# Performance work log

Hardware: AMD Instinct MI355X
Metric: run time of the kernel (lower is better)

The kernel has to match this reference:

```python
import jax, jax.numpy as jnp
import numpy as np

SIM_THRESHOLD = 0.7
EPS = 1e-8  # matches torch F.cosine_similarity eps

Q, M, D, C = 4096, 65536, 384, 128


def setup_inputs() -> dict:
    key = jax.random.key(0)
    k1, k2, k3 = jax.random.split(key, 3)
    query_embeddings = jax.random.normal(k1, (Q, D), dtype=jnp.float32)
    memory_embeddings = jax.random.normal(k2, (M, D), dtype=jnp.float32)
    # per-example one-hot-ish label vectors [M, C]
    memory_labels = jax.random.uniform(k3, (M, C), dtype=jnp.float32)
    return {
        "query_embeddings": query_embeddings,
        "memory_embeddings": memory_embeddings,
        "memory_labels": memory_labels,
    }


def _l2_normalize(x):
    n = jnp.sqrt(jnp.sum(x * x, axis=-1, keepdims=True))
    return x / jnp.maximum(n, EPS)


def reference(query_embeddings, memory_embeddings, memory_labels):
    # cosine similarity matrix [Q, M] via normalized GEMM
    qn = _l2_normalize(query_embeddings)          # [Q, D]
    mn = _l2_normalize(memory_embeddings)         # [M, D]
    sims = jnp.einsum("qd,md->qm", qn, mn)        # [Q, M]
    max_sim = jnp.max(sims, axis=1)               # [Q]
    max_idx = jnp.argmax(sims, axis=1)            # [Q]
    picked = memory_labels[max_idx]               # [Q, C] gather
    C_ = memory_labels.shape[1]
    uniform = jnp.full((1, C_), 1.0 / C_, dtype=picked.dtype)
    predictions = jnp.where((max_sim > SIM_THRESHOLD)[:, None], picked, uniform)
    return predictions
```

## Files before the change

### kernel.cpp

```cpp
#include <hip/hip_runtime.h>
#include <math.h>

#define QN 4096
#define MN 65536
#define DN 384
#define CN 128
#define NCHUNK 64
#define MROWS_PER_CHUNK (MN / NCHUNK)
#define MT_PER (MROWS_PER_CHUNK / 64)
#define BTILE_B (64 * DN)
#define NBUF 2

typedef __attribute__((ext_vector_type(8))) int i32x8;
typedef __attribute__((ext_vector_type(4))) int i32x4;
typedef __attribute__((ext_vector_type(4))) float f32x4;

__device__ __forceinline__ void async16(const void* g, void* l) {
  __builtin_amdgcn_global_load_lds(
      (const __attribute__((address_space(1))) unsigned int*)g,
      (__attribute__((address_space(3))) unsigned int*)l, 16, 0, 0);
}

__global__ __launch_bounds__(256) void nrm_kernel(const float* __restrict__ qe,
                                                  const float* __restrict__ me,
                                                  unsigned char* __restrict__ yq,
                                                  unsigned char* __restrict__ ym) {
  const int row = blockIdx.x * 4 + (threadIdx.x >> 6);
  const int lane = threadIdx.x & 63;
  const float* xr;
  unsigned char* yr;
  if (row < QN) {
    xr = qe + (size_t)row * DN;
    yr = yq + (size_t)row * DN;
  } else {
    xr = me + (size_t)(row - QN) * DN;
    yr = ym + (size_t)(row - QN) * DN;
  }
  float2 v[3];
  float ss = 0.f;
#pragma unroll
  for (int i = 0; i < 3; ++i) {
    v[i] = *(const float2*)&xr[lane * 2 + i * 128];
    ss += v[i].x * v[i].x + v[i].y * v[i].y;
  }
#pragma unroll
  for (int m = 1; m < 64; m <<= 1) ss += __shfl_xor(ss, m);
  const float scale = 1.0f / fmaxf(sqrtf(ss), 1e-8f);
  unsigned short* yw = (unsigned short*)yr;
#pragma unroll
  for (int i = 0; i < 3; ++i) {
    const int p = __builtin_amdgcn_cvt_pk_fp8_f32(v[i].x * scale,
                                                  v[i].y * scale, 0, false);
    yw[lane + i * 64] = (unsigned short)(p & 0xffff);
  }
}

__global__ __launch_bounds__(256, 2) void gemm_max_kernel(
    const unsigned char* __restrict__ qn8, const unsigned char* __restrict__ mn8,
    float* __restrict__ pmax) {
  __shared__ unsigned char Bs[NBUF * BTILE_B];
  __shared__ float smax[2][128];

  const int tid = threadIdx.x;
  const int wave = tid >> 6, lane = tid & 63;
  const int wr = wave >> 1, wc = wave & 1;
  const int quad = lane >> 4, l16 = lane & 15;
  const int r7 = l16 & 7;

  const int bid = blockIdx.y * gridDim.x + blockIdx.x;
  const int xcd = bid & 7;
  const int j = bid >> 3;
  const int ychunk = (xcd << 3) | (j >> 5);
  const int qrow0 = (j & 31) * 128;
  const int mchunk0 = ychunk * MROWS_PER_CHUNK;

  float rmax[16];
#pragma unroll
  for (int i = 0; i < 16; ++i) rmax[i] = -3.0e38f;

  {
    const unsigned char* abase = qn8 + (size_t)qrow0 * DN;
#pragma unroll
    for (int i = 0; i < 12; ++i) {
      const int ci = i * 256 + tid;
      const int row = ci / 24;
      const int jj = ci - row * 24;
      const int gj = (jj & 24) | ((jj ^ row) & 7);
      async16(abase + row * DN + gj * 16, &Bs[(i * 256 + wave * 64) * 16]);
    }
  }
  __syncthreads();
  i32x8 afr[3][4];
#pragma unroll
  for (int kc = 0; kc < 3; ++kc)
#pragma unroll
    for (int rt = 0; rt < 4; ++rt) {
      const unsigned char* p = &Bs[(wr * 64 + rt * 16 + l16) * DN];
      i32x4 lo = *(const i32x4*)&p[(kc * 8 + ((quad * 2 + 0) ^ r7)) * 16];
      i32x4 hi = *(const i32x4*)&p[(kc * 8 + ((quad * 2 + 1) ^ r7)) * 16];
      afr[kc][rt][0] = lo[0]; afr[kc][rt][1] = lo[1];
      afr[kc][rt][2] = lo[2]; afr[kc][rt][3] = lo[3];
      afr[kc][rt][4] = hi[0]; afr[kc][rt][5] = hi[1];
      afr[kc][rt][6] = hi[2]; afr[kc][rt][7] = hi[3];
    }
  __syncthreads();

  int srcoff[6];
#pragma unroll
  for (int i = 0; i < 6; ++i) {
    const int ci = i * 256 + tid;
    const int row = ci / 24;
    const int jj = ci - row * 24;
    const int gj = (jj & 24) | ((jj ^ row) & 7);
    srcoff[i] = row * DN + gj * 16;
  }

  const unsigned char* bchunk = mn8 + (size_t)mchunk0 * DN;
#pragma unroll
  for (int i = 0; i < 6; ++i)
    async16(bchunk + srcoff[i], &Bs[(i * 256 + wave * 64) * 16]);

#pragma unroll 1
  for (int mt = 0; mt < MT_PER; ++mt) {
    asm volatile("s_waitcnt vmcnt(0)" ::: "memory");
    __builtin_amdgcn_s_barrier();
    __builtin_amdgcn_sched_barrier(0);

    const unsigned char* cur = &Bs[(mt & 1) * BTILE_B];

    i32x8 bfr[3][2];
#pragma unroll
    for (int kc = 0; kc < 3; ++kc)
#pragma unroll
      for (int ct = 0; ct < 2; ++ct) {
        const unsigned char* p = &cur[(wc * 32 + ct * 16 + l16) * DN];
        i32x4 lo = *(const i32x4*)&p[(kc * 8 + ((quad * 2 + 0) ^ r7)) * 16];
        i32x4 hi = *(const i32x4*)&p[(kc * 8 + ((quad * 2 + 1) ^ r7)) * 16];
        bfr[kc][ct][0] = lo[0]; bfr[kc][ct][1] = lo[1];
        bfr[kc][ct][2] = lo[2]; bfr[kc][ct][3] = lo[3];
        bfr[kc][ct][4] = hi[0]; bfr[kc][ct][5] = hi[1];
        bfr[kc][ct][6] = hi[2]; bfr[kc][ct][7] = hi[3];
      }

    if (mt + 1 < MT_PER) {
      unsigned char* dst = &Bs[((mt + 1) & 1) * BTILE_B];
      const unsigned char* nb = bchunk + (size_t)(mt + 1) * BTILE_B;
#pragma unroll
      for (int i = 0; i < 6; ++i)
        async16(nb + srcoff[i], &dst[(i * 256 + wave * 64) * 16]);
    }

    f32x4 acc[4][2];
#pragma unroll
    for (int rt = 0; rt < 4; ++rt)
#pragma unroll
      for (int ct = 0; ct < 2; ++ct) acc[rt][ct] = (f32x4){0.f, 0.f, 0.f, 0.f};

    __builtin_amdgcn_s_setprio(1);
#pragma unroll
    for (int kc = 0; kc < 3; ++kc)
#pragma unroll
      for (int rt = 0; rt < 4; ++rt)
#pragma unroll
        for (int ct = 0; ct < 2; ++ct)
          acc[rt][ct] = __builtin_amdgcn_mfma_scale_f32_16x16x128_f8f6f4(
              afr[kc][rt], bfr[kc][ct], acc[rt][ct], 0, 0,
              0, 0x7f7f7f7f, 0, 0x7f7f7f7f);
    __builtin_amdgcn_s_setprio(0);

#pragma unroll
    for (int rt = 0; rt < 4; ++rt)
#pragma unroll
      for (int r = 0; r < 4; ++r) {
        const float v = fmaxf(acc[rt][0][r], acc[rt][1][r]);
        rmax[rt * 4 + r] = fmaxf(rmax[rt * 4 + r], v);
      }
  }

#pragma unroll
  for (int i = 0; i < 16; ++i) {
    float v = rmax[i];
    v = fmaxf(v, __shfl_xor(v, 1));
    v = fmaxf(v, __shfl_xor(v, 2));
    v = fmaxf(v, __shfl_xor(v, 4));
    v = fmaxf(v, __shfl_xor(v, 8));
    rmax[i] = v;
  }
  if (l16 == 0) {
#pragma unroll
    for (int rt = 0; rt < 4; ++rt)
#pragma unroll
      for (int r = 0; r < 4; ++r)
        smax[wc][wr * 64 + rt * 16 + quad * 4 + r] = rmax[rt * 4 + r];
  }
  __syncthreads();
  if (tid < 128) {
    const float v = fmaxf(smax[0][tid], smax[1][tid]);
    pmax[(size_t)(qrow0 + tid) * NCHUNK + ychunk] = v;
  }
}

__global__ __launch_bounds__(256) void decide_kernel(
    const float* __restrict__ pmax, const float* __restrict__ qe,
    const float* __restrict__ me, const float* __restrict__ labels,
    float* __restrict__ out) {
  const int q = blockIdx.x;
  const int t = threadIdx.x;
  __shared__ float smx;
  if (t < 64) {
    float v = pmax[(size_t)q * NCHUNK + t];
#pragma unroll
    for (int m = 1; m < 64; m <<= 1) v = fmaxf(v, __shfl_xor(v, m));
    if (t == 0) smx = v;
  }
  __syncthreads();
  if (smx <= 0.5f) {
    if (t < CN) out[(size_t)q * CN + t] = 1.0f / 128.0f;
    return;
  }
  __shared__ float sred[256];
  __shared__ int sidx[256];
  __shared__ float wsum[4];
  const float* qr = qe + (size_t)q * DN;
  float ss = 0.f;
  for (int i = t; i < DN; i += 256) ss += qr[i] * qr[i];
#pragma unroll
  for (int m = 1; m < 64; m <<= 1) ss += __shfl_xor(ss, m);
  if ((t & 63) == 0) wsum[t >> 6] = ss;
  __syncthreads();
  const float qnorm = fmaxf(sqrtf(wsum[0] + wsum[1] + wsum[2] + wsum[3]), 1e-8f);

  float best = -3.0e38f;
  int bidx = 0x7fffffff;
  for (int j = t; j < MN; j += 256) {
    const float* mr = me + (size_t)j * DN;
    float dot = 0.f, ms = 0.f;
    for (int k = 0; k < DN; ++k) {
      float a = qr[k], b = mr[k];
      dot += a * b;
      ms += b * b;
    }
    const float sim = dot / (qnorm * fmaxf(sqrtf(ms), 1e-8f));
    if (sim > best) { best = sim; bidx = j; }
  }
  sred[t] = best;
  sidx[t] = bidx;
  __syncthreads();
  for (int s = 128; s > 0; s >>= 1) {
    if (t < s) {
      const float ov = sred[t + s];
      const int oi = sidx[t + s];
      if (ov > sred[t] || (ov == sred[t] && oi < sidx[t])) {
        sred[t] = ov;
        sidx[t] = oi;
      }
    }
    __syncthreads();
  }
  const float mx = sred[0];
  const int mi = sidx[0];
  if (t < CN)
    out[(size_t)q * CN + t] =
        (mx > 0.7f) ? labels[(size_t)mi * CN + t] : (1.0f / 128.0f);
}

extern "C" void kernel_launch(void* const* d_in, const int* in_sizes, int n_in,
                              void* d_out, int out_size, void* d_ws,
                              size_t ws_size, hipStream_t stream) {
  const float* qe = (const float*)d_in[0];
  const float* me = (const float*)d_in[1];
  const float* lb = (const float*)d_in[2];
  float* out = (float*)d_out;

  char* ws = (char*)d_ws;
  const size_t OFF_QN = 0;
  const size_t OFF_MN = OFF_QN + (size_t)QN * DN;
  const size_t OFF_PMAX = OFF_MN + (size_t)MN * DN;
  unsigned char* qn8 = (unsigned char*)(ws + OFF_QN);
  unsigned char* mn8 = (unsigned char*)(ws + OFF_MN);
  float* pmax = (float*)(ws + OFF_PMAX);

  nrm_kernel<<<(QN + MN) / 4, 256, 0, stream>>>(qe, me, qn8, mn8);
  gemm_max_kernel<<<dim3(QN / 128, NCHUNK), 256, 0, stream>>>(qn8, mn8, pmax);
  decide_kernel<<<QN, 256, 0, stream>>>(pmax, qe, me, lb, out);
}
```

Baseline: 245.5 us.

## Give each wave a private triple-buffered B pipeline without block barriers

Each wave now streams only the 32 memory rows it consumes, in 16-row pieces, into its own three-slot LDS ring. It waits with vmcnt and lgkmcnt counters instead of a block-wide barrier each tile, and double-buffers the B fragments in registers so the next piece's LDS reads overlap the current MFMAs. This removes per-tile __syncthreads stalls and deepens prefetch. In exchange the MFMA batch per wait is smaller, B fragment reuse across column tiles drops, and LDS use changes from 48KB to 72KB, which could limit two blocks per CU.

```diff
diff --git a/kernel.cpp b/kernel.cpp
--- a/kernel.cpp
+++ b/kernel.cpp
@@ -9,7 +9,9 @@
 #define MROWS_PER_CHUNK (MN / NCHUNK)
 #define MT_PER (MROWS_PER_CHUNK / 64)
 #define BTILE_B (64 * DN)
-#define NBUF 2
+#define PIECE_B (16 * DN)
+#define NPBUF 3
+#define WBUF_B (NPBUF * PIECE_B)
 
 typedef __attribute__((ext_vector_type(8))) int i32x8;
 typedef __attribute__((ext_vector_type(4))) int i32x4;
@@ -58,7 +60,7 @@
 __global__ __launch_bounds__(256, 2) void gemm_max_kernel(
     const unsigned char* __restrict__ qn8, const unsigned char* __restrict__ mn8,
     float* __restrict__ pmax) {
-  __shared__ unsigned char Bs[NBUF * BTILE_B];
+  __shared__ unsigned char Bs[4 * WBUF_B];
   __shared__ float smax[2][128];
 
   const int tid = threadIdx.x;
@@ -105,77 +107,102 @@
     }
   __syncthreads();
 
-  int srcoff[6];
+  int srcw[6];
 #pragma unroll
   for (int i = 0; i < 6; ++i) {
-    const int ci = i * 256 + tid;
+    const int ci = i * 64 + lane;
     const int row = ci / 24;
     const int jj = ci - row * 24;
     const int gj = (jj & 24) | ((jj ^ row) & 7);
-    srcoff[i] = row * DN + gj * 16;
-  }
-
-  const unsigned char* bchunk = mn8 + (size_t)mchunk0 * DN;
-#pragma unroll
-  for (int i = 0; i < 6; ++i)
-    async16(bchunk + srcoff[i], &Bs[(i * 256 + wave * 64) * 16]);
+    srcw[i] = row * DN + gj * 16;
+  }
+  const unsigned char* bwave = mn8 + (size_t)(mchunk0 + wc * 32) * DN;
+  unsigned char* wbuf = &Bs[wave * WBUF_B];
+
+#pragma unroll
+  for (int q = 0; q < 3; ++q) {
+    const unsigned char* pb =
+        bwave + (size_t)(q >> 1) * BTILE_B + (size_t)(q & 1) * PIECE_B;
+#pragma unroll
+    for (int i = 0; i < 6; ++i)
+      async16(pb + srcw[i], wbuf + q * PIECE_B + i * 1024);
+  }
+
+  asm volatile("s_waitcnt vmcnt(12)" ::: "memory");
+  __builtin_amdgcn_sched_barrier(0);
+
+  i32x8 bfrA[3], bfrB[3];
+#pragma unroll
+  for (int kc = 0; kc < 3; ++kc) {
+    const unsigned char* pp = wbuf;
+    i32x4 lo =
+        *(const i32x4*)&pp[l16 * DN + (kc * 8 + ((quad * 2 + 0) ^ r7)) * 16];
+    i32x4 hi =
+        *(const i32x4*)&pp[l16 * DN + (kc * 8 + ((quad * 2 + 1) ^ r7)) * 16];
+    bfrA[kc][0] = lo[0]; bfrA[kc][1] = lo[1];
+    bfrA[kc][2] = lo[2]; bfrA[kc][3] = lo[3];
+    bfrA[kc][4] = hi[0]; bfrA[kc][5] = hi[1];
+    bfrA[kc][6] = hi[2]; bfrA[kc][7] = hi[3];
+  }
+
+  int b0 = 0;
+
+#define PIECE_BODY(P, CUR, NXT)                                                \
+  do {                                                                         \
+    const int p_ = (P);                                                        \
+    const int rb_ = (b0 == 2) ? 0 : b0 + 1;              \
+    if (p_ < 31) {                                                             \
+      if (p_ < 30)                                                             \
+        asm volatile("s_waitcnt vmcnt(6)" ::: "memory");                       \
+      else                                                                     \
+        asm volatile("s_waitcnt vmcnt(0)" ::: "memory");                       \
+      __builtin_amdgcn_sched_barrier(0);                                       \
+      const unsigned char* pp = wbuf + rb_ * PIECE_B;                          \
+      _Pragma("unroll") for (int kc = 0; kc < 3; ++kc) {                       \
+        i32x4 lo = *(const i32x4*)&pp[l16 * DN +                               \
+                                      (kc * 8 + ((quad * 2 + 0) ^ r7)) * 16];  \
+        i32x4 hi = *(const i32x4*)&pp[l16 * DN +                               \
+                                      (kc * 8 + ((quad * 2 + 1) ^ r7)) * 16];  \
+        NXT[kc][0] = lo[0]; NXT[kc][1] = lo[1];                                \
+        NXT[kc][2] = lo[2]; NXT[kc][3] = lo[3];                                \
+        NXT[kc][4] = hi[0]; NXT[kc][5] = hi[1];                                \
+        NXT[kc][6] = hi[2]; NXT[kc][7] = hi[3];                                \
+      }                                                                        \
+      asm volatile("s_waitcnt lgkmcnt(6)" ::: "memory");                       \
+    } else {                                                                   \
+      asm volatile("s_waitcnt lgkmcnt(0)" ::: "memory");                       \
+    }                                                                          \
+    __builtin_amdgcn_sched_barrier(0);                                         \
+    if (p_ + 3 < 32) {                                                         \
+      const int q_ = p_ + 3;                                                   \
+      const unsigned char* nb = bwave + (size_t)(q_ >> 1) * BTILE_B +          \
+                                (size_t)(q_ & 1) * PIECE_B;                    \
+      unsigned char* dst = wbuf + b0 * PIECE_B;                                \
+      _Pragma("unroll") for (int i = 0; i < 6; ++i)                            \
+          async16(nb + srcw[i], dst + i * 1024);                               \
+    }                                                                          \
+    f32x4 acc[4];                                                              \
+    _Pragma("unroll") for (int rt = 0; rt < 4; ++rt)                           \
+        acc[rt] = (f32x4){0.f, 0.f, 0.f, 0.f};                                 \
+    __builtin_amdgcn_s_setprio(1);                                             \
+    _Pragma("unroll") for (int kc = 0; kc < 3; ++kc)                           \
+        _Pragma("unroll") for (int rt = 0; rt < 4; ++rt)                       \
+            acc[rt] = __builtin_amdgcn_mfma_scale_f32_16x16x128_f8f6f4(        \
+                afr[kc][rt], CUR[kc], acc[rt], 0, 0, 0, 0x7f7f7f7f, 0,         \
+                0x7f7f7f7f);                                                   \
+    __builtin_amdgcn_s_setprio(0);                                             \
+    _Pragma("unroll") for (int rt = 0; rt < 4; ++rt)                           \
+        _Pragma("unroll") for (int r = 0; r < 4; ++r)                          \
+            rmax[rt * 4 + r] = fmaxf(rmax[rt * 4 + r], acc[rt][r]);            \
+    b0 = rb_;                                                                  \
+  } while (0)
 
 #pragma unroll 1
-  for (int mt = 0; mt < MT_PER; ++mt) {
-    asm volatile("s_waitcnt vmcnt(0)" ::: "memory");
-    __builtin_amdgcn_s_barrier();
-    __builtin_amdgcn_sched_barrier(0);
-
-    const unsigned char* cur = &Bs[(mt & 1) * BTILE_B];
-
-    i32x8 bfr[3][2];
-#pragma unroll
-    for (int kc = 0; kc < 3; ++kc)
-#pragma unroll
-      for (int ct = 0; ct < 2; ++ct) {
-        const unsigned char* p = &cur[(wc * 32 + ct * 16 + l16) * DN];
-        i32x4 lo = *(const i32x4*)&p[(kc * 8 + ((quad * 2 + 0) ^ r7)) * 16];
-        i32x4 hi = *(const i32x4*)&p[(kc * 8 + ((quad * 2 + 1) ^ r7)) * 16];
-        bfr[kc][ct][0] = lo[0]; bfr[kc][ct][1] = lo[1];
-        bfr[kc][ct][2] = lo[2]; bfr[kc][ct][3] = lo[3];
-        bfr[kc][ct][4] = hi[0]; bfr[kc][ct][5] = hi[1];
-        bfr[kc][ct][6] = hi[2]; bfr[kc][ct][7] = hi[3];
-      }
-
-    if (mt + 1 < MT_PER) {
-      unsigned char* dst = &Bs[((mt + 1) & 1) * BTILE_B];
-      const unsigned char* nb = bchunk + (size_t)(mt + 1) * BTILE_B;
-#pragma unroll
-      for (int i = 0; i < 6; ++i)
-        async16(nb + srcoff[i], &dst[(i * 256 + wave * 64) * 16]);
-    }
-
-    f32x4 acc[4][2];
-#pragma unroll
-    for (int rt = 0; rt < 4; ++rt)
-#pragma unroll
-      for (int ct = 0; ct < 2; ++ct) acc[rt][ct] = (f32x4){0.f, 0.f, 0.f, 0.f};
-
-    __builtin_amdgcn_s_setprio(1);
-#pragma unroll
-    for (int kc = 0; kc < 3; ++kc)
-#pragma unroll
-      for (int rt = 0; rt < 4; ++rt)
-#pragma unroll
-        for (int ct = 0; ct < 2; ++ct)
-          acc[rt][ct] = __builtin_amdgcn_mfma_scale_f32_16x16x128_f8f6f4(
-              afr[kc][rt], bfr[kc][ct], acc[rt][ct], 0, 0,
-              0, 0x7f7f7f7f, 0, 0x7f7f7f7f);
-    __builtin_amdgcn_s_setprio(0);
-
-#pragma unroll
-    for (int rt = 0; rt < 4; ++rt)
-#pragma unroll
-      for (int r = 0; r < 4; ++r) {
-        const float v = fmaxf(acc[rt][0][r], acc[rt][1][r]);
-        rmax[rt * 4 + r] = fmaxf(rmax[rt * 4 + r], v);
-      }
-  }
+  for (int pp2 = 0; pp2 < 32; pp2 += 2) {
+    PIECE_BODY(pp2, bfrA, bfrB);
+    PIECE_BODY(pp2 + 1, bfrB, bfrA);
+  }
+#undef PIECE_BODY
 
 #pragma unroll
   for (int i = 0; i < 16; ++i) {
```

Measured after the change: 265.9 us. 8.3% more time.

## Pre-swizzle memory embeddings into MFMA fragment layout and load B directly

Applied to the files above, without the earlier changes.

The normalization kernel now writes the fp8 memory embeddings in a fragment-major layout that matches the MFMA B-operand register layout. The GEMM kernel reads B fragments straight from global memory into registers with 32-byte loads, so it no longer stages B through LDS with a double buffer and per-tile barriers. This removes LDS traffic and synchronisation from the inner loop. In exchange, global loads are no longer prefetched asynchronously and their latency is exposed unless occupancy hides it, and the two column waves each read their own B data with no sharing through LDS.

```diff
diff --git a/kernel.cpp b/kernel.cpp
--- a/kernel.cpp
+++ b/kernel.cpp
@@ -8,8 +8,9 @@
 #define NCHUNK 64
 #define MROWS_PER_CHUNK (MN / NCHUNK)
 #define MT_PER (MROWS_PER_CHUNK / 64)
-#define BTILE_B (64 * DN)
-#define NBUF 2
+#define FRAG_B 2048
+#define GSTRIDE (3 * FRAG_B)
+#define TSTRIDE (4 * GSTRIDE)
 
 typedef __attribute__((ext_vector_type(8))) int i32x8;
 typedef __attribute__((ext_vector_type(4))) int i32x4;
@@ -27,15 +28,8 @@
                                                   unsigned char* __restrict__ ym) {
   const int row = blockIdx.x * 4 + (threadIdx.x >> 6);
   const int lane = threadIdx.x & 63;
-  const float* xr;
-  unsigned char* yr;
-  if (row < QN) {
-    xr = qe + (size_t)row * DN;
-    yr = yq + (size_t)row * DN;
-  } else {
-    xr = me + (size_t)(row - QN) * DN;
-    yr = ym + (size_t)(row - QN) * DN;
-  }
+  const float* xr = (row < QN) ? qe + (size_t)row * DN
+                               : me + (size_t)(row - QN) * DN;
   float2 v[3];
   float ss = 0.f;
 #pragma unroll
@@ -46,19 +40,33 @@
 #pragma unroll
   for (int m = 1; m < 64; m <<= 1) ss += __shfl_xor(ss, m);
   const float scale = 1.0f / fmaxf(sqrtf(ss), 1e-8f);
-  unsigned short* yw = (unsigned short*)yr;
-#pragma unroll
-  for (int i = 0; i < 3; ++i) {
-    const int p = __builtin_amdgcn_cvt_pk_fp8_f32(v[i].x * scale,
-                                                  v[i].y * scale, 0, false);
-    yw[lane + i * 64] = (unsigned short)(p & 0xffff);
+  if (row < QN) {
+    unsigned short* yw = (unsigned short*)(yq + (size_t)row * DN);
+#pragma unroll
+    for (int i = 0; i < 3; ++i) {
+      const int p = __builtin_amdgcn_cvt_pk_fp8_f32(v[i].x * scale,
+                                                    v[i].y * scale, 0, false);
+      yw[lane + i * 64] = (unsigned short)(p & 0xffff);
+    }
+  } else {
+    const int mr = row - QN;
+    const int g = mr >> 4, r15 = mr & 15;
+    const int fl = ((lane >> 4) << 4) + r15;
+    unsigned short* yw = (unsigned short*)ym;
+#pragma unroll
+    for (int i = 0; i < 3; ++i) {
+      const int p = __builtin_amdgcn_cvt_pk_fp8_f32(v[i].x * scale,
+                                                    v[i].y * scale, 0, false);
+      yw[((size_t)(g * 3 + i) * 64 + fl) * 16 + (lane & 15)] =
+          (unsigned short)(p & 0xffff);
+    }
   }
 }
 
 __global__ __launch_bounds__(256, 2) void gemm_max_kernel(
     const unsigned char* __restrict__ qn8, const unsigned char* __restrict__ mn8,
     float* __restrict__ pmax) {
-  __shared__ unsigned char Bs[NBUF * BTILE_B];
+  __shared__ unsigned char As[128 * DN];
   __shared__ float smax[2][128];
 
   const int tid = threadIdx.x;
@@ -86,7 +94,7 @@
       const int row = ci / 24;
       const int jj = ci - row * 24;
       const int gj = (jj & 24) | ((jj ^ row) & 7);
-      async16(abase + row * DN + gj * 16, &Bs[(i * 256 + wave * 64) * 16]);
+      async16(abase + row * DN + gj * 16, &As[(i * 256 + wave * 64) * 16]);
     }
   }
   __syncthreads();
@@ -95,7 +103,7 @@
   for (int kc = 0; kc < 3; ++kc)
 #pragma unroll
     for (int rt = 0; rt < 4; ++rt) {
-      const unsigned char* p = &Bs[(wr * 64 + rt * 16 + l16) * DN];
+      const unsigned char* p = &As[(wr * 64 + rt * 16 + l16) * DN];
       i32x4 lo = *(const i32x4*)&p[(kc * 8 + ((quad * 2 + 0) ^ r7)) * 16];
       i32x4 hi = *(const i32x4*)&p[(kc * 8 + ((quad * 2 + 1) ^ r7)) * 16];
       afr[kc][rt][0] = lo[0]; afr[kc][rt][1] = lo[1];
@@ -103,51 +111,18 @@
       afr[kc][rt][4] = hi[0]; afr[kc][rt][5] = hi[1];
       afr[kc][rt][6] = hi[2]; afr[kc][rt][7] = hi[3];
     }
-  __syncthreads();
-
-  int srcoff[6];
-#pragma unroll
-  for (int i = 0; i < 6; ++i) {
-    const int ci = i * 256 + tid;
-    const int row = ci / 24;
-    const int jj = ci - row * 24;
-    const int gj = (jj & 24) | ((jj ^ row) & 7);
-    srcoff[i] = row * DN + gj * 16;
-  }
-
-  const unsigned char* bchunk = mn8 + (size_t)mchunk0 * DN;
-#pragma unroll
-  for (int i = 0; i < 6; ++i)
-    async16(bchunk + srcoff[i], &Bs[(i * 256 + wave * 64) * 16]);
+
+  const int g0 = (mchunk0 >> 4) + wc * 2;
+  const unsigned char* bp0 = mn8 + ((size_t)g0 * 3 * 64 + lane) * 32;
+  const unsigned char* bp1 = bp0 + GSTRIDE;
 
 #pragma unroll 1
   for (int mt = 0; mt < MT_PER; ++mt) {
-    asm volatile("s_waitcnt vmcnt(0)" ::: "memory");
-    __builtin_amdgcn_s_barrier();
-    __builtin_amdgcn_sched_barrier(0);
-
-    const unsigned char* cur = &Bs[(mt & 1) * BTILE_B];
-
     i32x8 bfr[3][2];
 #pragma unroll
-    for (int kc = 0; kc < 3; ++kc)
-#pragma unroll
-      for (int ct = 0; ct < 2; ++ct) {
-        const unsigned char* p = &cur[(wc * 32 + ct * 16 + l16) * DN];
-        i32x4 lo = *(const i32x4*)&p[(kc * 8 + ((quad * 2 + 0) ^ r7)) * 16];
-        i32x4 hi = *(const i32x4*)&p[(kc * 8 + ((quad * 2 + 1) ^ r7)) * 16];
-        bfr[kc][ct][0] = lo[0]; bfr[kc][ct][1] = lo[1];
-        bfr[kc][ct][2] = lo[2]; bfr[kc][ct][3] = lo[3];
-        bfr[kc][ct][4] = hi[0]; bfr[kc][ct][5] = hi[1];
-        bfr[kc][ct][6] = hi[2]; bfr[kc][ct][7] = hi[3];
-      }
-
-    if (mt + 1 < MT_PER) {
-      unsigned char* dst = &Bs[((mt + 1) & 1) * BTILE_B];
-      const unsigned char* nb = bchunk + (size_t)(mt + 1) * BTILE_B;
-#pragma unroll
-      for (int i = 0; i < 6; ++i)
-        async16(nb + srcoff[i], &dst[(i * 256 + wave * 64) * 16]);
+    for (int kc = 0; kc < 3; ++kc) {
+      bfr[kc][0] = *(const i32x8*)(bp0 + kc * FRAG_B);
+      bfr[kc][1] = *(const i32x8*)(bp1 + kc * FRAG_B);
     }
 
     f32x4 acc[4][2];
@@ -175,6 +150,9 @@
         const float v = fmaxf(acc[rt][0][r], acc[rt][1][r]);
         rmax[rt * 4 + r] = fmaxf(rmax[rt * 4 + r], v);
       }
+
+    bp0 += TSTRIDE;
+    bp1 += TSTRIDE;
   }
 
 #pragma unroll
```

Result: slower. 252.1 us (+2.7%).
